# Optimization experiments

Hardware: AMD Instinct MI355X
Metric: run time of the kernel (lower is better)

Reference implementation:

```python
import jax, jax.numpy as jnp
import numpy as np
from jax import lax

# Physical / solver constants (from init_kwargs / module defaults)
G_OVER_L = 10.0
L1 = 1.0
L2 = 1.0
DT = 0.02
FRICTION = 0.1
EPS = 1e-5            # finite-difference step used by hamiltonian_gradients_numerical
TORQUE_IDX = 1        # acrobot: torque applied to joint 2
STATE_DIM = 2
# cost weights (not visible in truncated source; fixed named constants)
W_POS_1 = 1.0; W_POS_2 = 1.0
W_VEL_1 = 1.0; W_VEL_2 = 1.0
W_U = 0.01
W_TERM_POS = 10.0; W_TERM_VEL = 1.0

PI = 3.141592653589793
TWO_PI = 6.283185307179586


def angle_normalize(theta):
    return (theta + PI) % TWO_PI - PI


def hamiltonian(qp):
    # qp: (..., 4) = [q1, q2, p1, p2]
    q1, q2, p1, p2 = qp[..., 0], qp[..., 1], qp[..., 2], qp[..., 3]
    dq = q1 - q2
    denom = 2.0 * (1.0 + jnp.sin(dq) ** 2)
    T = (p1 ** 2 + 2.0 * p2 ** 2 - 2.0 * p1 * p2 * jnp.cos(dq)) / denom
    V = G_OVER_L * (L1 * (1.0 - jnp.cos(q1)) + L2 * (1.0 - jnp.cos(q2)))
    return T + V


def ham_grads(qp):
    # Central finite differences, vectorized over the 4 perturbation dims.
    eye = (EPS * jnp.eye(4, dtype=qp.dtype))          # [4,4]
    qp_plus = qp[..., None, :] + eye                   # (...,4,4)
    qp_minus = qp[..., None, :] - eye
    dH = (hamiltonian(qp_plus) - hamiltonian(qp_minus)) / (2.0 * EPS)  # (...,4)
    return dH[..., :STATE_DIM], dH[..., STATE_DIM:]


def symplectic_step(q, q_p, a):
    # q, q_p: [n, 2]; a: [n]
    qp = jnp.concatenate([q, q_p], axis=-1)
    dH_dq, dH_dp = ham_grads(qp)
    p_half = q_p - 0.5 * DT * dH_dq - 0.5 * DT * FRICTION * dH_dp
    _, dH_dp_mid = ham_grads(jnp.concatenate([q, p_half], axis=-1))
    q_new = q + DT * dH_dp_mid
    dH_dq_end, dH_dp_end = ham_grads(jnp.concatenate([q_new, p_half], axis=-1))
    p_new = p_half - 0.5 * DT * dH_dq_end - 0.5 * DT * FRICTION * dH_dp_end
    p_new = p_new.at[..., TORQUE_IDX].add(a * DT)
    return q_new, p_new


def rollout(q0, p0, actions):
    # actions: [n, T] -> scan over time
    def scan_fn(carry, a_t):
        q, p = carry
        q, p = symplectic_step(q, p, a_t)
        return (q, p), (q, p)

    _, (qs, ps) = lax.scan(scan_fn, (q0, p0), jnp.swapaxes(actions, 0, 1))
    # prepend initial state: [n, T+1, 2]
    q_traj = jnp.concatenate([q0[:, None, :], jnp.swapaxes(qs, 0, 1)], axis=1)
    p_traj = jnp.concatenate([p0[:, None, :], jnp.swapaxes(ps, 0, 1)], axis=1)
    return q_traj, p_traj


def trajectory_cost(q_traj, p_traj, actions, target_state):
    T = actions.shape[1]
    target = target_state[None, None, :]                    # [1,1,2]
    err = angle_normalize(q_traj[:, :T, :] - target)        # [n,T,2]
    pos_cost = W_POS_1 * err[..., 0] ** 2 + W_POS_2 * err[..., 1] ** 2
    vel_cost = W_VEL_1 * p_traj[:, :T, 0] ** 2 + W_VEL_2 * p_traj[:, :T, 1] ** 2
    control_cost = W_U * actions ** 2
    running = (pos_cost + vel_cost + control_cost).sum(axis=-1)
    err_term = angle_normalize(q_traj[:, -1, :] - target_state[None, :])
    vel_term = p_traj[:, -1, :]
    terminal = W_TERM_POS * (err_term ** 2).sum(-1) + W_TERM_VEL * (vel_term ** 2).sum(-1)
    return running + terminal


def setup_inputs() -> dict:
    key = jax.random.key(0)
    k1, k2, k3, k4 = jax.random.split(key, 4)
    n, T = 200000, 100
    return {
        "q0": jax.random.normal(k1, (n, 2), dtype=jnp.float32),
        "p0": jax.random.normal(k2, (n, 2), dtype=jnp.float32),
        "actions": jax.random.normal(k3, (n, T), dtype=jnp.float32),
        "target_state": jax.random.normal(k4, (2,), dtype=jnp.float32),
    }


def reference(q0, p0, actions, target_state):
    q_traj, p_traj = rollout(q0, p0, actions)
    return trajectory_cost(q_traj, p_traj, actions, target_state)
```

## Files before the change

kernel.cpp:

```cpp
#include <hip/hip_runtime.h>
#include <cmath>

#pragma clang fp contract(off)

#define PI_F     3.141592653589793f
#define TWOPI_F  6.283185307179586f
#define EPS_F    1e-5f
#define TWOEPS_F 2e-5f

__device__ __forceinline__ void gl_sincos(float y, float& sout, float& cout) {
    const double hpi_inv = 0x1.45F306DC9C883p+23;
    const double hpi     = 0x1.921FB54442D18p+0;
    const double ps1 = -0x1.555545995a603p-3;
    const double ps2 =  0x1.1107605230bc4p-7;
    const double ps3 = -0x1.994eb3774cf24p-13;
    const double pc1 = -0x1.ffffffd0c621cp-2;
    const double pc2 =  0x1.55553e1068f19p-5;
    const double pc3 = -0x1.6c087e89a359dp-10;
    const double pc4 =  0x1.99343027bf8c3p-16;

    double x = (double)y;
    double r = x * hpi_inv;
    int n = ((int)r + 0x800000) >> 24;
    double xr = x - (double)n * hpi;
    double x2 = xr * xr;

    double x3 = xr * x2;
    double s1 = ps2 + x2 * ps3;
    double x7 = x3 * x2;
    double ss = xr + x3 * ps1;
    double psin = ss + x7 * s1;

    double x4 = x2 * x2;
    double c2 = pc3 + x2 * pc4;
    double c1 = 1.0 + x2 * pc1;
    double x6 = x4 * x2;
    double cc = c1 + x4 * pc2;
    double pcos = cc + x6 * c2;

    float psin_f = (float)psin;
    float pcos_f = (float)pcos;
    float s_sel = (n & 1) ? pcos_f : psin_f;
    float c_sel = (n & 1) ? psin_f : pcos_f;
    sout = (n & 2) ? -s_sel : s_sel;
    cout = ((n + 1) & 2) ? -c_sel : c_sel;
}

__device__ __forceinline__ float gl_cosf(float y) {
    float s, c;
    gl_sincos(y, s, c);
    return c;
}

__device__ __forceinline__ float angnorm(float x) {
    float t = x + PI_F;
    float r = fmodf(t, TWOPI_F);
    if (r < 0.0f) r += TWOPI_F;
    return r - PI_F;
}

__device__ __forceinline__ float ham_eval(float p1, float p2,
                                          float sdq, float cdq,
                                          float c1, float c2) {
    float denom = 2.0f * __builtin_fmaf(sdq, sdq, 1.0f);
    float B  = 2.0f * (p2 * p2);
    float AB = __builtin_fmaf(p1, p1, B);
    float t  = (2.0f * p1) * p2;
    float num = __builtin_fmaf(-t, cdq, AB);
    float T = num / denom;
    float VV = (1.0f - c1) + (1.0f - c2);
    return __builtin_fmaf(10.0f, VV, T);
}

struct QTrig {
    float sdq, cdq, c1, c2;
    float sa, ca, c1p;
    float sb, cb, c1m;
    float sc, cc, c2p;
    float sd, cd, c2m;
};

__device__ __forceinline__ void qtrig_all(float q1, float q2, QTrig& t) {
    gl_sincos(q1 - q2, t.sdq, t.cdq);
    t.c1 = gl_cosf(q1);
    t.c2 = gl_cosf(q2);
    float q1p = q1 + EPS_F, q1m = q1 - EPS_F;
    gl_sincos(q1p - q2, t.sa, t.ca);  t.c1p = gl_cosf(q1p);
    gl_sincos(q1m - q2, t.sb, t.cb);  t.c1m = gl_cosf(q1m);
    float q2p = q2 + EPS_F, q2m = q2 - EPS_F;
    gl_sincos(q1 - q2p, t.sc, t.cc);  t.c2p = gl_cosf(q2p);
    gl_sincos(q1 - q2m, t.sd, t.cd);  t.c2m = gl_cosf(q2m);
}

__device__ __forceinline__ void grads_full(const QTrig& t, float p1, float p2,
                                           float& dHq1, float& dHq2,
                                           float& dHp1, float& dHp2) {
    {
        float Hp = ham_eval(p1, p2, t.sa, t.ca, t.c1p, t.c2);
        float Hm = ham_eval(p1, p2, t.sb, t.cb, t.c1m, t.c2);
        dHq1 = (Hp - Hm) / TWOEPS_F;
    }
    {
        float Hp = ham_eval(p1, p2, t.sc, t.cc, t.c1, t.c2p);
        float Hm = ham_eval(p1, p2, t.sd, t.cd, t.c1, t.c2m);
        dHq2 = (Hp - Hm) / TWOEPS_F;
    }
    {
        float Hp = ham_eval(p1 + EPS_F, p2, t.sdq, t.cdq, t.c1, t.c2);
        float Hm = ham_eval(p1 - EPS_F, p2, t.sdq, t.cdq, t.c1, t.c2);
        dHp1 = (Hp - Hm) / TWOEPS_F;
    }
    {
        float Hp = ham_eval(p1, p2 + EPS_F, t.sdq, t.cdq, t.c1, t.c2);
        float Hm = ham_eval(p1, p2 - EPS_F, t.sdq, t.cdq, t.c1, t.c2);
        dHp2 = (Hp - Hm) / TWOEPS_F;
    }
}

__device__ __forceinline__ void grads_p(const QTrig& t, float p1, float p2,
                                        float& dHp1, float& dHp2) {
    {
        float Hp = ham_eval(p1 + EPS_F, p2, t.sdq, t.cdq, t.c1, t.c2);
        float Hm = ham_eval(p1 - EPS_F, p2, t.sdq, t.cdq, t.c1, t.c2);
        dHp1 = (Hp - Hm) / TWOEPS_F;
    }
    {
        float Hp = ham_eval(p1, p2 + EPS_F, t.sdq, t.cdq, t.c1, t.c2);
        float Hm = ham_eval(p1, p2 - EPS_F, t.sdq, t.cdq, t.c1, t.c2);
        dHp2 = (Hp - Hm) / TWOEPS_F;
    }
}

__global__ __launch_bounds__(256)
void mpc_rollout_kernel(const float* __restrict__ q0,
                        const float* __restrict__ p0,
                        const float* __restrict__ actions,
                        const float* __restrict__ target,
                        float* __restrict__ out,
                        int n, int T) {
    int i = blockIdx.x * blockDim.x + threadIdx.x;
    if (i >= n) return;

    float q1 = q0[2 * i],  q2 = q0[2 * i + 1];
    float p1 = p0[2 * i],  p2 = p0[2 * i + 1];
    float tg1 = target[0], tg2 = target[1];
    const float* act = actions + (size_t)i * (size_t)T;

    float running = 0.0f;

    QTrig qt;
    qtrig_all(q1, q2, qt);

#pragma unroll 1
    for (int ts = 0; ts < T; ++ts) {
        float a = act[ts];

        {
            float e1 = angnorm(q1 - tg1);
            float e2 = angnorm(q2 - tg2);
            float pos = __builtin_fmaf(e1, e1, e2 * e2);
            float vel = __builtin_fmaf(p1, p1, p2 * p2);
            float c = __builtin_fmaf(0.01f, a * a, pos + vel);
            running += c;
        }

        float dq1g, dq2g, dp1g, dp2g;
        grads_full(qt, p1, p2, dq1g, dq2g, dp1g, dp2g);

        float ph1 = __builtin_fmaf(-0.001f, dp1g, __builtin_fmaf(-0.01f, dq1g, p1));
        float ph2 = __builtin_fmaf(-0.001f, dp2g, __builtin_fmaf(-0.01f, dq2g, p2));

        float dpm1, dpm2;
        grads_p(qt, ph1, ph2, dpm1, dpm2);

        float qn1 = __builtin_fmaf(0.02f, dpm1, q1);
        float qn2 = __builtin_fmaf(0.02f, dpm2, q2);

        qtrig_all(qn1, qn2, qt);
        float dq1e, dq2e, dp1e, dp2e;
        grads_full(qt, ph1, ph2, dq1e, dq2e, dp1e, dp2e);

        float pn1 = __builtin_fmaf(-0.001f, dp1e, __builtin_fmaf(-0.01f, dq1e, ph1));
        float pn2 = __builtin_fmaf(-0.001f, dp2e, __builtin_fmaf(-0.01f, dq2e, ph2));
        pn2 = __builtin_fmaf(a, 0.02f, pn2);

        q1 = qn1; q2 = qn2; p1 = pn1; p2 = pn2;
    }

    float e1 = angnorm(q1 - tg1);
    float e2 = angnorm(q2 - tg2);
    float S  = __builtin_fmaf(e2, e2, e1 * e1);
    float S2 = __builtin_fmaf(p2, p2, p1 * p1);
    float term = __builtin_fmaf(10.0f, S, S2);

    out[i] = running + term;
}

extern "C" void kernel_launch(void* const* d_in, const int* in_sizes, int n_in,
                              void* d_out, int out_size, void* d_ws, size_t ws_size,
                              hipStream_t stream) {
    const float* q0      = (const float*)d_in[0];
    const float* p0      = (const float*)d_in[1];
    const float* actions = (const float*)d_in[2];
    const float* target  = (const float*)d_in[3];
    float* out = (float*)d_out;

    int n = in_sizes[0] / 2;
    int T = in_sizes[2] / n;

    int block = 256;
    int grid = (n + block - 1) / block;
    mpc_rollout_kernel<<<grid, block, 0, stream>>>(q0, p0, actions, target, out, n, T);
}
```

Before: 702.1 us.

## Precompute per-q Hamiltonian terms and pack finite differences into float2 math

Moves the denominators and potential terms that depend only on position into qtrig_all, so each finite-difference evaluation no longer recomputes them. The plus and minus perturbations are evaluated as paired float2 ops, which can map to packed FMA/mul instructions on CDNA. fmodf in angnorm is replaced by a multiply-floor reduction with correction steps. This cuts redundant ALU work in the hot loop, but packed division may still lower to scalar sequences and the new angle reduction could differ in rounding at edge cases.

Result: faster. 685.3 us (-2.4%).

```diff
diff --git a/kernel.cpp b/kernel.cpp
--- a/kernel.cpp
+++ b/kernel.cpp
@@ -7,6 +7,12 @@
 #define TWOPI_F  6.283185307179586f
 #define EPS_F    1e-5f
 #define TWOEPS_F 2e-5f
+
+typedef float v2f __attribute__((ext_vector_type(2)));
+
+__device__ __forceinline__ v2f pk_fma(v2f a, v2f b, v2f c) {
+    return __builtin_elementwise_fma(a, b, c);
+}
 
 __device__ __forceinline__ void gl_sincos(float y, float& sout, float& cout) {
     const double hpi_inv = 0x1.45F306DC9C883p+23;
@@ -53,82 +59,102 @@
 }
 
 __device__ __forceinline__ float angnorm(float x) {
+    const double inv_twopi = 1.0 / (double)TWOPI_F;
     float t = x + PI_F;
-    float r = fmodf(t, TWOPI_F);
+    int k = (int)((double)t * inv_twopi);
+    float r = __builtin_fmaf((float)(-k), TWOPI_F, t);
+    if (r >= TWOPI_F)  r -= TWOPI_F;
+    if (r <= -TWOPI_F) r += TWOPI_F;
     if (r < 0.0f) r += TWOPI_F;
     return r - PI_F;
 }
 
-__device__ __forceinline__ float ham_eval(float p1, float p2,
-                                          float sdq, float cdq,
-                                          float c1, float c2) {
-    float denom = 2.0f * __builtin_fmaf(sdq, sdq, 1.0f);
-    float B  = 2.0f * (p2 * p2);
-    float AB = __builtin_fmaf(p1, p1, B);
-    float t  = (2.0f * p1) * p2;
-    float num = __builtin_fmaf(-t, cdq, AB);
-    float T = num / denom;
-    float VV = (1.0f - c1) + (1.0f - c2);
-    return __builtin_fmaf(10.0f, VV, T);
-}
-
 struct QTrig {
-    float sdq, cdq, c1, c2;
-    float sa, ca, c1p;
-    float sb, cb, c1m;
-    float sc, cc, c2p;
-    float sd, cd, c2m;
+    float cdq, den0, vv0;
+    v2f c_q1, den_q1, vv_q1;
+    v2f c_q2, den_q2, vv_q2;
 };
 
 __device__ __forceinline__ void qtrig_all(float q1, float q2, QTrig& t) {
-    gl_sincos(q1 - q2, t.sdq, t.cdq);
-    t.c1 = gl_cosf(q1);
-    t.c2 = gl_cosf(q2);
+    float sdq, cdq, c1v, c2v;
+    gl_sincos(q1 - q2, sdq, cdq);
+    c1v = gl_cosf(q1);
+    c2v = gl_cosf(q2);
     float q1p = q1 + EPS_F, q1m = q1 - EPS_F;
-    gl_sincos(q1p - q2, t.sa, t.ca);  t.c1p = gl_cosf(q1p);
-    gl_sincos(q1m - q2, t.sb, t.cb);  t.c1m = gl_cosf(q1m);
+    float sa, ca, sb, cb;
+    gl_sincos(q1p - q2, sa, ca);
+    gl_sincos(q1m - q2, sb, cb);
+    float c1p = gl_cosf(q1p);
+    float c1m = gl_cosf(q1m);
     float q2p = q2 + EPS_F, q2m = q2 - EPS_F;
-    gl_sincos(q1 - q2p, t.sc, t.cc);  t.c2p = gl_cosf(q2p);
-    gl_sincos(q1 - q2m, t.sd, t.cd);  t.c2m = gl_cosf(q2m);
+    float sc, cc, sd, cd;
+    gl_sincos(q1 - q2p, sc, cc);
+    gl_sincos(q1 - q2m, sd, cd);
+    float c2p = gl_cosf(q2p);
+    float c2m = gl_cosf(q2m);
+
+    float w1 = 1.0f - c1v;
+    float w2 = 1.0f - c2v;
+    t.cdq  = cdq;
+    t.den0 = 2.0f * __builtin_fmaf(sdq, sdq, 1.0f);
+    t.vv0  = w1 + w2;
+
+    t.c_q1 = (v2f){ca, cb};
+    v2f s1 = (v2f){sa, sb};
+    t.den_q1 = 2.0f * pk_fma(s1, s1, (v2f){1.0f, 1.0f});
+    t.vv_q1  = ((v2f){1.0f, 1.0f} - (v2f){c1p, c1m}) + w2;
+
+    t.c_q2 = (v2f){cc, cd};
+    v2f s2 = (v2f){sc, sd};
+    t.den_q2 = 2.0f * pk_fma(s2, s2, (v2f){1.0f, 1.0f});
+    t.vv_q2  = w1 + ((v2f){1.0f, 1.0f} - (v2f){c2p, c2m});
+}
+
+__device__ __forceinline__ float fd_q(float AB, float tt, v2f c, v2f den, v2f vv) {
+    v2f num = pk_fma((v2f){-tt, -tt}, c, (v2f){AB, AB});
+    v2f T = num / den;
+    v2f H = pk_fma((v2f){10.0f, 10.0f}, vv, T);
+    return (H.x - H.y) / TWOEPS_F;
+}
+
+__device__ __forceinline__ float fd_p1(const QTrig& t, float p1, float p2) {
+    v2f p1v = (v2f){p1, p1} + (v2f){EPS_F, -EPS_F};
+    float B = 2.0f * (p2 * p2);
+    v2f AB = pk_fma(p1v, p1v, (v2f){B, B});
+    v2f tp = (2.0f * p1v) * p2;
+    v2f num = pk_fma(-tp, (v2f){t.cdq, t.cdq}, AB);
+    v2f T = num / (v2f){t.den0, t.den0};
+    v2f H = pk_fma((v2f){10.0f, 10.0f}, (v2f){t.vv0, t.vv0}, T);
+    return (H.x - H.y) / TWOEPS_F;
+}
+
+__device__ __forceinline__ float fd_p2(const QTrig& t, float p1, float p2) {
+    v2f p2v = (v2f){p2, p2} + (v2f){EPS_F, -EPS_F};
+    v2f B = 2.0f * (p2v * p2v);
+    v2f AB = pk_fma((v2f){p1, p1}, (v2f){p1, p1}, B);
+    v2f tp = (2.0f * p1) * p2v;
+    v2f num = pk_fma(-tp, (v2f){t.cdq, t.cdq}, AB);
+    v2f T = num / (v2f){t.den0, t.den0};
+    v2f H = pk_fma((v2f){10.0f, 10.0f}, (v2f){t.vv0, t.vv0}, T);
+    return (H.x - H.y) / TWOEPS_F;
 }
 
 __device__ __forceinline__ void grads_full(const QTrig& t, float p1, float p2,
                                            float& dHq1, float& dHq2,
                                            float& dHp1, float& dHp2) {
-    {
-        float Hp = ham_eval(p1, p2, t.sa, t.ca, t.c1p, t.c2);
-        float Hm = ham_eval(p1, p2, t.sb, t.cb, t.c1m, t.c2);
-        dHq1 = (Hp - Hm) / TWOEPS_F;
-    }
-    {
-        float Hp = ham_eval(p1, p2, t.sc, t.cc, t.c1, t.c2p);
-        float Hm = ham_eval(p1, p2, t.sd, t.cd, t.c1, t.c2m);
-        dHq2 = (Hp - Hm) / TWOEPS_F;
-    }
-    {
-        float Hp = ham_eval(p1 + EPS_F, p2, t.sdq, t.cdq, t.c1, t.c2);
-        float Hm = ham_eval(p1 - EPS_F, p2, t.sdq, t.cdq, t.c1, t.c2);
-        dHp1 = (Hp - Hm) / TWOEPS_F;
-    }
-    {
-        float Hp = ham_eval(p1, p2 + EPS_F, t.sdq, t.cdq, t.c1, t.c2);
-        float Hm = ham_eval(p1, p2 - EPS_F, t.sdq, t.cdq, t.c1, t.c2);
-        dHp2 = (Hp - Hm) / TWOEPS_F;
-    }
+    float B  = 2.0f * (p2 * p2);
+    float AB = __builtin_fmaf(p1, p1, B);
+    float tt = (2.0f * p1) * p2;
+    dHq1 = fd_q(AB, tt, t.c_q1, t.den_q1, t.vv_q1);
+    dHq2 = fd_q(AB, tt, t.c_q2, t.den_q2, t.vv_q2);
+    dHp1 = fd_p1(t, p1, p2);
+    dHp2 = fd_p2(t, p1, p2);
 }
 
 __device__ __forceinline__ void grads_p(const QTrig& t, float p1, float p2,
                                         float& dHp1, float& dHp2) {
-    {
-        float Hp = ham_eval(p1 + EPS_F, p2, t.sdq, t.cdq, t.c1, t.c2);
-        float Hm = ham_eval(p1 - EPS_F, p2, t.sdq, t.cdq, t.c1, t.c2);
-        dHp1 = (Hp - Hm) / TWOEPS_F;
-    }
-    {
-        float Hp = ham_eval(p1, p2 + EPS_F, t.sdq, t.cdq, t.c1, t.c2);
-        float Hm = ham_eval(p1, p2 - EPS_F, t.sdq, t.cdq, t.c1, t.c2);
-        dHp2 = (Hp - Hm) / TWOEPS_F;
-    }
+    dHp1 = fd_p1(t, p1, p2);
+    dHp2 = fd_p2(t, p1, p2);
 }
 
 __global__ __launch_bounds__(256)
@@ -167,24 +193,27 @@
         float dq1g, dq2g, dp1g, dp2g;
         grads_full(qt, p1, p2, dq1g, dq2g, dp1g, dp2g);
 
-        float ph1 = __builtin_fmaf(-0.001f, dp1g, __builtin_fmaf(-0.01f, dq1g, p1));
-        float ph2 = __builtin_fmaf(-0.001f, dp2g, __builtin_fmaf(-0.01f, dq2g, p2));
+        v2f pv  = (v2f){p1, p2};
+        v2f dqg = (v2f){dq1g, dq2g};
+        v2f dpg = (v2f){dp1g, dp2g};
+        v2f ph  = pk_fma((v2f){-0.001f, -0.001f}, dpg,
+                         pk_fma((v2f){-0.01f, -0.01f}, dqg, pv));
 
         float dpm1, dpm2;
-        grads_p(qt, ph1, ph2, dpm1, dpm2);
-
-        float qn1 = __builtin_fmaf(0.02f, dpm1, q1);
-        float qn2 = __builtin_fmaf(0.02f, dpm2, q2);
-
-        qtrig_all(qn1, qn2, qt);
+        grads_p(qt, ph.x, ph.y, dpm1, dpm2);
+
+        v2f qv = (v2f){q1, q2};
+        v2f qn = pk_fma((v2f){0.02f, 0.02f}, (v2f){dpm1, dpm2}, qv);
+
+        qtrig_all(qn.x, qn.y, qt);
         float dq1e, dq2e, dp1e, dp2e;
-        grads_full(qt, ph1, ph2, dq1e, dq2e, dp1e, dp2e);
-
-        float pn1 = __builtin_fmaf(-0.001f, dp1e, __builtin_fmaf(-0.01f, dq1e, ph1));
-        float pn2 = __builtin_fmaf(-0.001f, dp2e, __builtin_fmaf(-0.01f, dq2e, ph2));
-        pn2 = __builtin_fmaf(a, 0.02f, pn2);
-
-        q1 = qn1; q2 = qn2; p1 = pn1; p2 = pn2;
+        grads_full(qt, ph.x, ph.y, dq1e, dq2e, dp1e, dp2e);
+
+        v2f pn = pk_fma((v2f){-0.001f, -0.001f}, (v2f){dp1e, dp2e},
+                        pk_fma((v2f){-0.01f, -0.01f}, (v2f){dq1e, dq2e}, ph));
+        float pn2 = __builtin_fmaf(a, 0.02f, pn.y);
+
+        q1 = qn.x; q2 = qn.y; p1 = pn.x; p2 = pn2;
     }
 
     float e1 = angnorm(q1 - tg1);
```
